# Kernel optimization log

Measured on AMD Instinct MI355X. Metric: run time of the kernel, lower is better.

The kernel has to match this reference:

```python
import jax, jax.numpy as jnp
import numpy as np

N = 100000
NFEAT = 512
NHID = 256
NCLASS = 40
E = 1600000
K = 10          # nlayers propagation hops
ALPHA = 0.1


def setup_inputs() -> dict:
    key = jax.random.key(0)
    ks = jax.random.split(key, 8)
    x = jax.random.normal(ks[0], (N, NFEAT), dtype=jnp.float32)
    edge_src = jax.random.randint(ks[1], (E,), 0, N, dtype=jnp.int32)
    edge_dst = jax.random.randint(ks[2], (E,), 0, N, dtype=jnp.int32)
    # roughly row-stochastic-scale edge values (avg degree ~16)
    edge_val = jax.random.uniform(ks[3], (E,), dtype=jnp.float32) * (1.0 / 16.0)
    stdv1 = 1.0 / np.sqrt(NFEAT)
    W1 = jax.random.uniform(ks[4], (NFEAT, NHID), minval=-stdv1, maxval=stdv1, dtype=jnp.float32)
    b1 = jax.random.uniform(ks[5], (NHID,), minval=-stdv1, maxval=stdv1, dtype=jnp.float32)
    stdv2 = 1.0 / np.sqrt(NHID)
    W2 = jax.random.uniform(ks[6], (NHID, NCLASS), minval=-stdv2, maxval=stdv2, dtype=jnp.float32)
    b2 = jax.random.uniform(ks[7], (NCLASS,), minval=-stdv2, maxval=stdv2, dtype=jnp.float32)
    return {"x": x, "edge_src": edge_src, "edge_dst": edge_dst, "edge_val": edge_val,
            "W1": W1, "b1": b1, "W2": W2, "b2": b2}


def _spmm(edge_src, edge_dst, edge_val, z):
    # sparse adj @ z via gather + segment-sum scatter: out[dst] += val * z[src]
    msgs = edge_val[:, None] * z[edge_src]          # [E, C]
    return jax.ops.segment_sum(msgs, edge_dst, num_segments=N)


def reference(x, edge_src, edge_dst, edge_val, W1, b1, W2, b2):
    # MLP transform (dropout is identity in eval mode)
    h = jax.nn.relu(x @ W1 + b1)                    # [N, NHID]
    h = h @ W2 + b2                                 # [N, NCLASS]
    # APPNP propagation: z <- (1-alpha) * A z + alpha * h
    def step(z, _):
        z = _spmm(edge_src, edge_dst, edge_val, z) * (1.0 - ALPHA) + ALPHA * h
        return z, None
    z, _ = jax.lax.scan(step, h, None, length=K)
    return jax.nn.log_softmax(z, axis=1)
```

## Files before the change

### kernel.cpp

```cpp
#include <hip/hip_runtime.h>
#include <hip/hip_bf16.h>
#include <math.h>

#define NN     100000
#define NFEATD 512
#define NHIDD  256
#define NCLS   40
#define NE     1600000
#define KHOP   10

typedef __attribute__((ext_vector_type(8))) short short8;
typedef __attribute__((ext_vector_type(4))) float floatx4;

static __device__ __forceinline__ float bf2f(unsigned int u) {
  unsigned int x = u << 16;
  float f;
  __builtin_memcpy(&f, &x, 4);
  return f;
}
static __device__ __forceinline__ unsigned short f2bf(float f) {
  unsigned int x;
  __builtin_memcpy(&x, &x, 0);
  __builtin_memcpy(&x, &f, 4);
  x = (x + 0x7fffu + ((x >> 16) & 1u)) >> 16;
  return (unsigned short)x;
}

__global__ __launch_bounds__(256) void wt_kernel(const float* __restrict__ W1,
                                                 unsigned short* __restrict__ Wt) {
  int i = blockIdx.x * 256 + threadIdx.x;
  int k = i >> 8;
  int n = i & 255;
  Wt[n * 512 + k] = f2bf(W1[i]);
}

__global__ __launch_bounds__(256) void gemm1_mfma_kernel(
    const float* __restrict__ x, const unsigned short* __restrict__ Wt,
    const float* __restrict__ b1, unsigned short* __restrict__ h1) {
  __shared__ unsigned short As[128 * 40];
  __shared__ unsigned short Bs[128 * 40];
  const int tid = threadIdx.x;
  const int lane = tid & 63;
  const int wave = tid >> 6;
  const int wr = wave >> 1, wc = wave & 1;
  const int m = lane & 15, quad = lane >> 4;
  const int c0 = blockIdx.x * 128;
  const int r0 = blockIdx.y * 128;

  const int arow = tid >> 3;
  const int akq = tid & 7;
  const int brow = tid >> 2;
  const int bkq = tid & 3;

  floatx4 acc[4][4];
#pragma unroll
  for (int i = 0; i < 4; ++i)
#pragma unroll
    for (int j = 0; j < 4; ++j) acc[i][j] = (floatx4){0.f, 0.f, 0.f, 0.f};

  float4 aR[4];
  uint4 bR[2];
#pragma unroll
  for (int rep = 0; rep < 4; ++rep) {
    int grow = r0 + arow + rep * 32;
    aR[rep] = make_float4(0.f, 0.f, 0.f, 0.f);
    if (grow < NN) aR[rep] = *(const float4*)(x + grow * NFEATD + akq * 4);
  }
#pragma unroll
  for (int rep = 0; rep < 2; ++rep)
    bR[rep] = *(const uint4*)(Wt + (c0 + brow + rep * 64) * NFEATD + bkq * 8);

  for (int kt = 0; kt < NFEATD; kt += 32) {
#pragma unroll
    for (int rep = 0; rep < 4; ++rep) {
      ushort4 o;
      o.x = f2bf(aR[rep].x);
      o.y = f2bf(aR[rep].y);
      o.z = f2bf(aR[rep].z);
      o.w = f2bf(aR[rep].w);
      *(ushort4*)&As[(arow + rep * 32) * 40 + akq * 4] = o;
    }
#pragma unroll
    for (int rep = 0; rep < 2; ++rep)
      *(uint4*)&Bs[(brow + rep * 64) * 40 + bkq * 8] = bR[rep];
    __syncthreads();

    int ktn = kt + 32;
    if (ktn < NFEATD) {
#pragma unroll
      for (int rep = 0; rep < 4; ++rep) {
        int grow = r0 + arow + rep * 32;
        float4 v = make_float4(0.f, 0.f, 0.f, 0.f);
        if (grow < NN) v = *(const float4*)(x + grow * NFEATD + ktn + akq * 4);
        aR[rep] = v;
      }
#pragma unroll
      for (int rep = 0; rep < 2; ++rep)
        bR[rep] = *(const uint4*)(Wt + (c0 + brow + rep * 64) * NFEATD + ktn + bkq * 8);
    }

    short8 af[4], bfr[4];
#pragma unroll
    for (int i = 0; i < 4; ++i)
      af[i] = *(const short8*)&As[(wr * 64 + i * 16 + m) * 40 + quad * 8];
#pragma unroll
    for (int j = 0; j < 4; ++j)
      bfr[j] = *(const short8*)&Bs[(wc * 64 + j * 16 + m) * 40 + quad * 8];
#pragma unroll
    for (int i = 0; i < 4; ++i)
#pragma unroll
      for (int j = 0; j < 4; ++j)
        acc[i][j] = __builtin_amdgcn_mfma_f32_16x16x32_bf16(af[i], bfr[j], acc[i][j], 0, 0, 0);
    __syncthreads();
  }

  float bias[4];
#pragma unroll
  for (int j = 0; j < 4; ++j) bias[j] = b1[c0 + wc * 64 + j * 16 + m];
#pragma unroll
  for (int i = 0; i < 4; ++i) {
#pragma unroll
    for (int r = 0; r < 4; ++r) {
      int row = r0 + wr * 64 + i * 16 + quad * 4 + r;
      if (row < NN) {
#pragma unroll
        for (int j = 0; j < 4; ++j) {
          float v = acc[i][j][r] + bias[j];
          h1[row * NHIDD + c0 + wc * 64 + j * 16 + m] = f2bf(fmaxf(v, 0.f));
        }
      }
    }
  }
}

__global__ __launch_bounds__(256) void gemm2_kernel(
    const unsigned short* __restrict__ h1, const float* __restrict__ W2,
    const float* __restrict__ b2, float* __restrict__ h) {
  __shared__ float w2s[NHIDD * NCLS];
  __shared__ float b2s[NCLS];
  __shared__ unsigned short h1s[64 * 264];
  const int tid = threadIdx.x;
  const int r0 = blockIdx.x * 64;
  for (int i = tid; i < NHIDD * NCLS; i += 256) w2s[i] = W2[i];
  if (tid < NCLS) b2s[tid] = b2[tid];
#pragma unroll
  for (int q = 0; q < 8; ++q) {
    int l = tid + q * 256;
    int lr = l >> 5;
    int lc = (l & 31) << 3;
    int row = r0 + lr;
    uint4 v = make_uint4(0, 0, 0, 0);
    if (row < NN) v = *(const uint4*)(h1 + row * NHIDD + lc);
    *(uint4*)&h1s[lr * 264 + lc] = v;
  }
  __syncthreads();
  const int lr = tid >> 2;
  const int cq = (tid & 3) * 10;
  float acc[10];
#pragma unroll
  for (int j = 0; j < 10; ++j) acc[j] = 0.f;
#pragma unroll 4
  for (int k = 0; k < NHIDD; k += 2) {
    unsigned int hp = *(const unsigned int*)&h1s[lr * 264 + k];
    float a0 = bf2f(hp & 0xffffu);
    float a1 = bf2f(hp >> 16);
    const float* w0 = &w2s[k * NCLS + cq];
    const float* w1 = &w2s[(k + 1) * NCLS + cq];
#pragma unroll
    for (int j = 0; j < 10; ++j)
      acc[j] = fmaf(a1, w1[j], fmaf(a0, w0[j], acc[j]));
  }
  int row = r0 + lr;
  if (row < NN) {
#pragma unroll
    for (int j = 0; j < 10; ++j) h[row * NCLS + cq + j] = acc[j] + b2s[cq + j];
  }
}

__global__ __launch_bounds__(256) void zero_kernel(int* __restrict__ p, int n) {
  int i = blockIdx.x * 256 + threadIdx.x;
  if (i < n) p[i] = 0;
}
__global__ __launch_bounds__(256) void count_kernel(const int* __restrict__ edst,
                                                    int* __restrict__ counts) {
  int e = blockIdx.x * 256 + threadIdx.x;
  if (e < NE) atomicAdd(&counts[edst[e]], 1);
}
__global__ __launch_bounds__(256) void scan_blocks_kernel(
    const int* __restrict__ counts, int* __restrict__ row_start,
    int* __restrict__ bsum) {
  __shared__ int s[256];
  int gid = blockIdx.x * 256 + threadIdx.x;
  int v = (gid < NN) ? counts[gid] : 0;
  s[threadIdx.x] = v;
  __syncthreads();
  for (int off = 1; off < 256; off <<= 1) {
    int t = (threadIdx.x >= off) ? s[threadIdx.x - off] : 0;
    __syncthreads();
    s[threadIdx.x] += t;
    __syncthreads();
  }
  if (gid < NN) row_start[gid + 1] = s[threadIdx.x];
  if (threadIdx.x == 255) bsum[blockIdx.x] = s[255];
}
#define NB 391
__global__ __launch_bounds__(512) void scan_sums_kernel(int* __restrict__ bsum) {
  __shared__ int s[512];
  int tid = threadIdx.x;
  int v = (tid < NB) ? bsum[tid] : 0;
  s[tid] = v;
  __syncthreads();
  for (int off = 1; off < 512; off <<= 1) {
    int t = (tid >= off) ? s[tid - off] : 0;
    __syncthreads();
    s[tid] += t;
    __syncthreads();
  }
  if (tid < NB) bsum[tid] = (tid == 0) ? 0 : s[tid - 1];
}
__global__ __launch_bounds__(256) void add_off_kernel(int* __restrict__ row_start,
                                                      const int* __restrict__ bsum) {
  int gid = blockIdx.x * 256 + threadIdx.x;
  if (gid < NN) row_start[gid + 1] += bsum[blockIdx.x];
  if (gid == 0) row_start[0] = 0;
}
__global__ __launch_bounds__(256) void scatter_kernel(
    const int* __restrict__ esrc, const int* __restrict__ edst,
    const float* __restrict__ eval, const int* __restrict__ row_start,
    int* __restrict__ cursor, int2* __restrict__ csr_pair) {
  int e = blockIdx.x * 256 + threadIdx.x;
  if (e < NE) {
    int d = edst[e];
    int p = atomicAdd(&cursor[d], 1);
    int idx = row_start[d] + p;
    csr_pair[idx] = make_int2(esrc[e], __float_as_int(eval[e]));
  }
}

__global__ __launch_bounds__(256) void prop_kernel(
    const int* __restrict__ row_start, const int2* __restrict__ csr_pair,
    const float* __restrict__ z, const float* __restrict__ h,
    float* __restrict__ zo) {
  int t = blockIdx.x * 256 + threadIdx.x;
  if (t >= NN * 10) return;
  unsigned int r = (unsigned int)t / 10u;
  int cg = t - (int)r * 10;
  const float* zc = z + cg * 4;
  int e0 = row_start[r], e1 = row_start[r + 1];
  float4 acc = make_float4(0.f, 0.f, 0.f, 0.f);
  int e = e0;
  for (; e + 4 <= e1; e += 4) {
    int2 p0 = csr_pair[e + 0];
    int2 p1 = csr_pair[e + 1];
    int2 p2 = csr_pair[e + 2];
    int2 p3 = csr_pair[e + 3];
    const float4 z0 = *(const float4*)(zc + p0.x * 40);
    const float4 z1 = *(const float4*)(zc + p1.x * 40);
    const float4 z2 = *(const float4*)(zc + p2.x * 40);
    const float4 z3 = *(const float4*)(zc + p3.x * 40);
    float v0 = __int_as_float(p0.y), v1 = __int_as_float(p1.y);
    float v2 = __int_as_float(p2.y), v3 = __int_as_float(p3.y);
    acc.x = fmaf(v0, z0.x, acc.x);
    acc.y = fmaf(v0, z0.y, acc.y);
    acc.z = fmaf(v0, z0.z, acc.z);
    acc.w = fmaf(v0, z0.w, acc.w);
    acc.x = fmaf(v1, z1.x, acc.x);
    acc.y = fmaf(v1, z1.y, acc.y);
    acc.z = fmaf(v1, z1.z, acc.z);
    acc.w = fmaf(v1, z1.w, acc.w);
    acc.x = fmaf(v2, z2.x, acc.x);
    acc.y = fmaf(v2, z2.y, acc.y);
    acc.z = fmaf(v2, z2.z, acc.z);
    acc.w = fmaf(v2, z2.w, acc.w);
    acc.x = fmaf(v3, z3.x, acc.x);
    acc.y = fmaf(v3, z3.y, acc.y);
    acc.z = fmaf(v3, z3.z, acc.z);
    acc.w = fmaf(v3, z3.w, acc.w);
  }
  for (; e < e1; ++e) {
    int2 p = csr_pair[e];
    float v = __int_as_float(p.y);
    const float4 zv = *(const float4*)(zc + p.x * 40);
    acc.x = fmaf(v, zv.x, acc.x);
    acc.y = fmaf(v, zv.y, acc.y);
    acc.z = fmaf(v, zv.z, acc.z);
    acc.w = fmaf(v, zv.w, acc.w);
  }
  const float4 hv = *(const float4*)(h + r * NCLS + cg * 4);
  float4 o;
  o.x = 0.9f * acc.x + 0.1f * hv.x;
  o.y = 0.9f * acc.y + 0.1f * hv.y;
  o.z = 0.9f * acc.z + 0.1f * hv.z;
  o.w = 0.9f * acc.w + 0.1f * hv.w;
  *(float4*)(zo + r * NCLS + cg * 4) = o;
}

__global__ __launch_bounds__(256) void lsm_kernel(float* __restrict__ zio) {
  int r = blockIdx.x * 256 + threadIdx.x;
  if (r >= NN) return;
  float v[NCLS];
#pragma unroll
  for (int q = 0; q < 10; ++q) {
    float4 t = *(const float4*)(zio + r * NCLS + q * 4);
    v[q * 4 + 0] = t.x;
    v[q * 4 + 1] = t.y;
    v[q * 4 + 2] = t.z;
    v[q * 4 + 3] = t.w;
  }
  float m = v[0];
#pragma unroll
  for (int i = 1; i < NCLS; ++i) m = fmaxf(m, v[i]);
  float ssum = 0.f;
#pragma unroll
  for (int i = 0; i < NCLS; ++i) ssum += expf(v[i] - m);
  float lse = m + logf(ssum);
#pragma unroll
  for (int q = 0; q < 10; ++q) {
    float4 t;
    t.x = v[q * 4 + 0] - lse;
    t.y = v[q * 4 + 1] - lse;
    t.z = v[q * 4 + 2] - lse;
    t.w = v[q * 4 + 3] - lse;
    *(float4*)(zio + r * NCLS + q * 4) = t;
  }
}

extern "C" void kernel_launch(void* const* d_in, const int* in_sizes, int n_in,
                              void* d_out, int out_size, void* d_ws, size_t ws_size,
                              hipStream_t stream) {
  const float* x = (const float*)d_in[0];
  const int* esrc = (const int*)d_in[1];
  const int* edst = (const int*)d_in[2];
  const float* eval = (const float*)d_in[3];
  const float* W1 = (const float*)d_in[4];
  const float* b1 = (const float*)d_in[5];
  const float* W2 = (const float*)d_in[6];
  const float* b2 = (const float*)d_in[7];
  float* out = (float*)d_out;
  char* ws = (char*)d_ws;

  float* h = (float*)(ws + 0);
  float* zA = (float*)(ws + 16000000);
  unsigned short* Wt = (unsigned short*)(ws + 16000000);
  unsigned short* h1 = (unsigned short*)(ws + 32000000);
  int* counts = (int*)(ws + 83200000);
  int* cursor = (int*)(ws + 83600000);
  int* row_start = (int*)(ws + 84000000);
  int* bsum = (int*)(ws + 84400640);
  int2* csr_pair = (int2*)(ws + 84402688);

  zero_kernel<<<(2 * NN + 255) / 256, 256, 0, stream>>>(counts, 2 * NN);

  wt_kernel<<<(NFEATD * NHIDD) / 256, 256, 0, stream>>>(W1, Wt);
  gemm1_mfma_kernel<<<dim3(2, (NN + 127) / 128), 256, 0, stream>>>(x, Wt, b1, h1);
  gemm2_kernel<<<(NN + 63) / 64, 256, 0, stream>>>(h1, W2, b2, h);

  count_kernel<<<(NE + 255) / 256, 256, 0, stream>>>(edst, counts);
  scan_blocks_kernel<<<NB, 256, 0, stream>>>(counts, row_start, bsum);
  scan_sums_kernel<<<1, 512, 0, stream>>>(bsum);
  add_off_kernel<<<NB, 256, 0, stream>>>(row_start, bsum);
  scatter_kernel<<<(NE + 255) / 256, 256, 0, stream>>>(esrc, edst, eval, row_start,
                                                       cursor, csr_pair);

  const float* zin = h;
  float* zout = zA;
  for (int i = 0; i < KHOP; ++i) {
    prop_kernel<<<(NN * 10 + 255) / 256, 256, 0, stream>>>(row_start, csr_pair,
                                                           zin, h, zout);
    if (i == 0) {
      zin = zA;
      zout = out;
    } else {
      float* t = (float*)zin;
      zin = zout;
      zout = t;
    }
  }

  lsm_kernel<<<(NN + 255) / 256, 256, 0, stream>>>(out);
}
```

Baseline: 1.158 ms.

## Store propagation features in bf16 and degree-sort rows for load balance

The propagation state z and the MLP output h are now stored as bf16 instead of fp32, which halves the bytes gathered per edge in each of the ten SpMM hops. Each thread now handles 8 classes with 16-byte loads, and the edge loop is unrolled by 8. Rows are bucketed by in-degree through a histogram and permutation, and the CSR is built in that sorted order, so neighbouring threads get similar edge counts and wave divergence drops. The cost is a few extra preprocessing kernels, plus bf16 rounding error that builds up across the hops.

```diff
diff --git a/kernel.cpp b/kernel.cpp
--- a/kernel.cpp
+++ b/kernel.cpp
@@ -20,10 +20,21 @@
 }
 static __device__ __forceinline__ unsigned short f2bf(float f) {
   unsigned int x;
-  __builtin_memcpy(&x, &x, 0);
   __builtin_memcpy(&x, &f, 4);
   x = (x + 0x7fffu + ((x >> 16) & 1u)) >> 16;
   return (unsigned short)x;
+}
+static __device__ __forceinline__ void bf8_to_f(const uint4 u, float* f) {
+  unsigned int a0 = u.x, a1 = u.y, a2 = u.z, a3 = u.w;
+  unsigned int t;
+  t = a0 << 16;          __builtin_memcpy(&f[0], &t, 4);
+  t = a0 & 0xffff0000u;  __builtin_memcpy(&f[1], &t, 4);
+  t = a1 << 16;          __builtin_memcpy(&f[2], &t, 4);
+  t = a1 & 0xffff0000u;  __builtin_memcpy(&f[3], &t, 4);
+  t = a2 << 16;          __builtin_memcpy(&f[4], &t, 4);
+  t = a2 & 0xffff0000u;  __builtin_memcpy(&f[5], &t, 4);
+  t = a3 << 16;          __builtin_memcpy(&f[6], &t, 4);
+  t = a3 & 0xffff0000u;  __builtin_memcpy(&f[7], &t, 4);
 }
 
 __global__ __launch_bounds__(256) void wt_kernel(const float* __restrict__ W1,
@@ -135,7 +146,7 @@
 
 __global__ __launch_bounds__(256) void gemm2_kernel(
     const unsigned short* __restrict__ h1, const float* __restrict__ W2,
-    const float* __restrict__ b2, float* __restrict__ h) {
+    const float* __restrict__ b2, unsigned short* __restrict__ hb) {
   __shared__ float w2s[NHIDD * NCLS];
   __shared__ float b2s[NCLS];
   __shared__ unsigned short h1s[64 * 264];
@@ -173,7 +184,11 @@
   int row = r0 + lr;
   if (row < NN) {
 #pragma unroll
-    for (int j = 0; j < 10; ++j) h[row * NCLS + cq + j] = acc[j] + b2s[cq + j];
+    for (int jj = 0; jj < 5; ++jj) {
+      unsigned int u = (unsigned int)f2bf(acc[2 * jj] + b2s[cq + 2 * jj]) |
+                       ((unsigned int)f2bf(acc[2 * jj + 1] + b2s[cq + 2 * jj + 1]) << 16);
+      *(unsigned int*)&hb[row * NCLS + cq + 2 * jj] = u;
+    }
   }
 }
 
@@ -186,12 +201,49 @@
   int e = blockIdx.x * 256 + threadIdx.x;
   if (e < NE) atomicAdd(&counts[edst[e]], 1);
 }
+__global__ __launch_bounds__(256) void hist_kernel(const int* __restrict__ counts,
+                                                   int* __restrict__ binoff) {
+  int r = blockIdx.x * 256 + threadIdx.x;
+  if (r < NN) {
+    int d = counts[r];
+    if (d > 63) d = 63;
+    atomicAdd(&binoff[d], 1);
+  }
+}
+__global__ __launch_bounds__(64) void binscan_kernel(int* __restrict__ binoff) {
+  __shared__ int s[64];
+  int t = threadIdx.x;
+  s[t] = binoff[t];
+  __syncthreads();
+  if (t == 0) {
+    int run = 0;
+    for (int i = 0; i < 64; ++i) {
+      int c = s[i];
+      s[i] = run;
+      run += c;
+    }
+  }
+  __syncthreads();
+  binoff[t] = s[t];
+}
+__global__ __launch_bounds__(256) void scatter_rows_kernel(
+    const int* __restrict__ counts, int* __restrict__ binoff,
+    int* __restrict__ perm, int* __restrict__ spos) {
+  int r = blockIdx.x * 256 + threadIdx.x;
+  if (r < NN) {
+    int d = counts[r];
+    if (d > 63) d = 63;
+    int pos = atomicAdd(&binoff[d], 1);
+    perm[pos] = r;
+    spos[r] = pos;
+  }
+}
 __global__ __launch_bounds__(256) void scan_blocks_kernel(
-    const int* __restrict__ counts, int* __restrict__ row_start,
-    int* __restrict__ bsum) {
+    const int* __restrict__ counts, const int* __restrict__ perm,
+    int* __restrict__ srs, int* __restrict__ bsum) {
   __shared__ int s[256];
   int gid = blockIdx.x * 256 + threadIdx.x;
-  int v = (gid < NN) ? counts[gid] : 0;
+  int v = (gid < NN) ? counts[perm[gid]] : 0;
   s[threadIdx.x] = v;
   __syncthreads();
   for (int off = 1; off < 256; off <<= 1) {
@@ -200,7 +252,7 @@
     s[threadIdx.x] += t;
     __syncthreads();
   }
-  if (gid < NN) row_start[gid + 1] = s[threadIdx.x];
+  if (gid < NN) srs[gid + 1] = s[threadIdx.x];
   if (threadIdx.x == 255) bsum[blockIdx.x] = s[255];
 }
 #define NB 391
@@ -218,94 +270,94 @@
   }
   if (tid < NB) bsum[tid] = (tid == 0) ? 0 : s[tid - 1];
 }
-__global__ __launch_bounds__(256) void add_off_kernel(int* __restrict__ row_start,
+__global__ __launch_bounds__(256) void add_off_kernel(int* __restrict__ srs,
                                                       const int* __restrict__ bsum) {
   int gid = blockIdx.x * 256 + threadIdx.x;
-  if (gid < NN) row_start[gid + 1] += bsum[blockIdx.x];
-  if (gid == 0) row_start[0] = 0;
+  if (gid < NN) srs[gid + 1] += bsum[blockIdx.x];
+  if (gid == 0) srs[0] = 0;
 }
 __global__ __launch_bounds__(256) void scatter_kernel(
     const int* __restrict__ esrc, const int* __restrict__ edst,
-    const float* __restrict__ eval, const int* __restrict__ row_start,
-    int* __restrict__ cursor, int2* __restrict__ csr_pair) {
+    const float* __restrict__ eval, const int* __restrict__ srs,
+    const int* __restrict__ spos, int* __restrict__ cursor,
+    int2* __restrict__ csr_pair) {
   int e = blockIdx.x * 256 + threadIdx.x;
   if (e < NE) {
-    int d = edst[e];
-    int p = atomicAdd(&cursor[d], 1);
-    int idx = row_start[d] + p;
+    int p = spos[edst[e]];
+    int idx = srs[p] + atomicAdd(&cursor[p], 1);
     csr_pair[idx] = make_int2(esrc[e], __float_as_int(eval[e]));
   }
 }
 
 __global__ __launch_bounds__(256) void prop_kernel(
-    const int* __restrict__ row_start, const int2* __restrict__ csr_pair,
-    const float* __restrict__ z, const float* __restrict__ h,
-    float* __restrict__ zo) {
+    const int* __restrict__ srs, const int* __restrict__ perm,
+    const int2* __restrict__ csr_pair, const unsigned short* __restrict__ zi,
+    const unsigned short* __restrict__ hb, unsigned short* __restrict__ zo) {
   int t = blockIdx.x * 256 + threadIdx.x;
-  if (t >= NN * 10) return;
-  unsigned int r = (unsigned int)t / 10u;
-  int cg = t - (int)r * 10;
-  const float* zc = z + cg * 4;
-  int e0 = row_start[r], e1 = row_start[r + 1];
-  float4 acc = make_float4(0.f, 0.f, 0.f, 0.f);
+  if (t >= NN * 5) return;
+  unsigned int p = (unsigned int)t / 5u;
+  int cg8 = (t - (int)p * 5) * 8;
+  int e0 = srs[p], e1 = srs[p + 1];
+  int r = perm[p];
+  float acc[8];
+#pragma unroll
+  for (int j = 0; j < 8; ++j) acc[j] = 0.f;
+
   int e = e0;
-  for (; e + 4 <= e1; e += 4) {
-    int2 p0 = csr_pair[e + 0];
-    int2 p1 = csr_pair[e + 1];
-    int2 p2 = csr_pair[e + 2];
-    int2 p3 = csr_pair[e + 3];
-    const float4 z0 = *(const float4*)(zc + p0.x * 40);
-    const float4 z1 = *(const float4*)(zc + p1.x * 40);
-    const float4 z2 = *(const float4*)(zc + p2.x * 40);
-    const float4 z3 = *(const float4*)(zc + p3.x * 40);
-    float v0 = __int_as_float(p0.y), v1 = __int_as_float(p1.y);
-    float v2 = __int_as_float(p2.y), v3 = __int_as_float(p3.y);
-    acc.x = fmaf(v0, z0.x, acc.x);
-    acc.y = fmaf(v0, z0.y, acc.y);
-    acc.z = fmaf(v0, z0.z, acc.z);
-    acc.w = fmaf(v0, z0.w, acc.w);
-    acc.x = fmaf(v1, z1.x, acc.x);
-    acc.y = fmaf(v1, z1.y, acc.y);
-    acc.z = fmaf(v1, z1.z, acc.z);
-    acc.w = fmaf(v1, z1.w, acc.w);
-    acc.x = fmaf(v2, z2.x, acc.x);
-    acc.y = fmaf(v2, z2.y, acc.y);
-    acc.z = fmaf(v2, z2.z, acc.z);
-    acc.w = fmaf(v2, z2.w, acc.w);
-    acc.x = fmaf(v3, z3.x, acc.x);
-    acc.y = fmaf(v3, z3.y, acc.y);
-    acc.z = fmaf(v3, z3.z, acc.z);
-    acc.w = fmaf(v3, z3.w, acc.w);
+  for (; e + 8 <= e1; e += 8) {
+    int2 pr[8];
+#pragma unroll
+    for (int q = 0; q < 8; ++q) pr[q] = csr_pair[e + q];
+    uint4 g[8];
+#pragma unroll
+    for (int q = 0; q < 8; ++q)
+      g[q] = *(const uint4*)(zi + pr[q].x * NCLS + cg8);
+#pragma unroll
+    for (int q = 0; q < 8; ++q) {
+      float zf[8];
+      bf8_to_f(g[q], zf);
+      float v = __int_as_float(pr[q].y);
+#pragma unroll
+      for (int j = 0; j < 8; ++j) acc[j] = fmaf(v, zf[j], acc[j]);
+    }
   }
   for (; e < e1; ++e) {
-    int2 p = csr_pair[e];
-    float v = __int_as_float(p.y);
-    const float4 zv = *(const float4*)(zc + p.x * 40);
-    acc.x = fmaf(v, zv.x, acc.x);
-    acc.y = fmaf(v, zv.y, acc.y);
-    acc.z = fmaf(v, zv.z, acc.z);
-    acc.w = fmaf(v, zv.w, acc.w);
-  }
-  const float4 hv = *(const float4*)(h + r * NCLS + cg * 4);
-  float4 o;
-  o.x = 0.9f * acc.x + 0.1f * hv.x;
-  o.y = 0.9f * acc.y + 0.1f * hv.y;
-  o.z = 0.9f * acc.z + 0.1f * hv.z;
-  o.w = 0.9f * acc.w + 0.1f * hv.w;
-  *(float4*)(zo + r * NCLS + cg * 4) = o;
-}
-
-__global__ __launch_bounds__(256) void lsm_kernel(float* __restrict__ zio) {
+    int2 pr = csr_pair[e];
+    uint4 g = *(const uint4*)(zi + pr.x * NCLS + cg8);
+    float zf[8];
+    bf8_to_f(g, zf);
+    float v = __int_as_float(pr.y);
+#pragma unroll
+    for (int j = 0; j < 8; ++j) acc[j] = fmaf(v, zf[j], acc[j]);
+  }
+
+  uint4 hu = *(const uint4*)(hb + r * NCLS + cg8);
+  float hf[8];
+  bf8_to_f(hu, hf);
+  uint4 o;
+  unsigned int w[4];
+#pragma unroll
+  for (int i = 0; i < 4; ++i) {
+    unsigned int lo = f2bf(0.9f * acc[2 * i] + 0.1f * hf[2 * i]);
+    unsigned int hi = f2bf(0.9f * acc[2 * i + 1] + 0.1f * hf[2 * i + 1]);
+    w[i] = lo | (hi << 16);
+  }
+  o.x = w[0];
+  o.y = w[1];
+  o.z = w[2];
+  o.w = w[3];
+  *(uint4*)(zo + r * NCLS + cg8) = o;
+}
+
+__global__ __launch_bounds__(256) void lsm_kernel(const unsigned short* __restrict__ zf,
+                                                  float* __restrict__ out) {
   int r = blockIdx.x * 256 + threadIdx.x;
   if (r >= NN) return;
   float v[NCLS];
 #pragma unroll
-  for (int q = 0; q < 10; ++q) {
-    float4 t = *(const float4*)(zio + r * NCLS + q * 4);
-    v[q * 4 + 0] = t.x;
-    v[q * 4 + 1] = t.y;
-    v[q * 4 + 2] = t.z;
-    v[q * 4 + 3] = t.w;
+  for (int q = 0; q < 5; ++q) {
+    uint4 u = *(const uint4*)(zf + r * NCLS + q * 8);
+    bf8_to_f(u, v + q * 8);
   }
   float m = v[0];
 #pragma unroll
@@ -316,12 +368,12 @@
   float lse = m + logf(ssum);
 #pragma unroll
   for (int q = 0; q < 10; ++q) {
-    float4 t;
-    t.x = v[q * 4 + 0] - lse;
-    t.y = v[q * 4 + 1] - lse;
-    t.z = v[q * 4 + 2] - lse;
-    t.w = v[q * 4 + 3] - lse;
-    *(float4*)(zio + r * NCLS + q * 4) = t;
+    float4 o;
+    o.x = v[q * 4 + 0] - lse;
+    o.y = v[q * 4 + 1] - lse;
+    o.z = v[q * 4 + 2] - lse;
+    o.w = v[q * 4 + 3] - lse;
+    *(float4*)(out + r * NCLS + q * 4) = o;
   }
 }
 
@@ -339,43 +391,51 @@
   float* out = (float*)d_out;
   char* ws = (char*)d_ws;
 
-  float* h = (float*)(ws + 0);
-  float* zA = (float*)(ws + 16000000);
-  unsigned short* Wt = (unsigned short*)(ws + 16000000);
-  unsigned short* h1 = (unsigned short*)(ws + 32000000);
-  int* counts = (int*)(ws + 83200000);
-  int* cursor = (int*)(ws + 83600000);
-  int* row_start = (int*)(ws + 84000000);
-  int* bsum = (int*)(ws + 84400640);
-  int2* csr_pair = (int2*)(ws + 84402688);
+  unsigned short* hb = (unsigned short*)(ws + 0);
+  unsigned short* zB0 = (unsigned short*)(ws + 8000000);
+  unsigned short* zB1 = (unsigned short*)(ws + 16000000);
+  unsigned short* Wt = (unsigned short*)(ws + 24000000);
+  unsigned short* h1 = (unsigned short*)(ws + 24400000);
+  int* counts = (int*)(ws + 75600000);
+  int* cursor = (int*)(ws + 76000000);
+  int* srs = (int*)(ws + 76400000);
+  int* bsum = (int*)(ws + 76800064);
+  int* binoff = (int*)(ws + 76802112);
+  int* perm = (int*)(ws + 76802624);
+  int* spos = (int*)(ws + 77202624);
+  int2* csr_pair = (int2*)(ws + 77602624);
 
   zero_kernel<<<(2 * NN + 255) / 256, 256, 0, stream>>>(counts, 2 * NN);
+  zero_kernel<<<1, 256, 0, stream>>>(binoff, 64);
 
   wt_kernel<<<(NFEATD * NHIDD) / 256, 256, 0, stream>>>(W1, Wt);
   gemm1_mfma_kernel<<<dim3(2, (NN + 127) / 128), 256, 0, stream>>>(x, Wt, b1, h1);
-  gemm2_kernel<<<(NN + 63) / 64, 256, 0, stream>>>(h1, W2, b2, h);
+  gemm2_kernel<<<(NN + 63) / 64, 256, 0, stream>>>(h1, W2, b2, hb);
 
   count_kernel<<<(NE + 255) / 256, 256, 0, stream>>>(edst, counts);
-  scan_blocks_kernel<<<NB, 256, 0, stream>>>(counts, row_start, bsum);
+  hist_kernel<<<(NN + 255) / 256, 256, 0, stream>>>(counts, binoff);
+  binscan_kernel<<<1, 64, 0, stream>>>(binoff);
+  scatter_rows_kernel<<<(NN + 255) / 256, 256, 0, stream>>>(counts, binoff, perm, spos);
+  scan_blocks_kernel<<<NB, 256, 0, stream>>>(counts, perm, srs, bsum);
   scan_sums_kernel<<<1, 512, 0, stream>>>(bsum);
-  add_off_kernel<<<NB, 256, 0, stream>>>(row_start, bsum);
-  scatter_kernel<<<(NE + 255) / 256, 256, 0, stream>>>(esrc, edst, eval, row_start,
+  add_off_kernel<<<NB, 256, 0, stream>>>(srs, bsum);
+  scatter_kernel<<<(NE + 255) / 256, 256, 0, stream>>>(esrc, edst, eval, srs, spos,
                                                        cursor, csr_pair);
 
-  const float* zin = h;
-  float* zout = zA;
+  const unsigned short* zin = hb;
+  unsigned short* zout = zB0;
   for (int i = 0; i < KHOP; ++i) {
-    prop_kernel<<<(NN * 10 + 255) / 256, 256, 0, stream>>>(row_start, csr_pair,
-                                                           zin, h, zout);
+    prop_kernel<<<(NN * 5 + 255) / 256, 256, 0, stream>>>(srs, perm, csr_pair,
+                                                          zin, hb, zout);
     if (i == 0) {
-      zin = zA;
-      zout = out;
+      zin = zB0;
+      zout = zB1;
     } else {
-      float* t = (float*)zin;
+      unsigned short* t = (unsigned short*)zin;
       zin = zout;
       zout = t;
     }
   }
 
-  lsm_kernel<<<(NN + 255) / 256, 256, 0, stream>>>(out);
-}
+  lsm_kernel<<<(NN + 255) / 256, 256, 0, stream>>>(zB1, out);
+}
```

Result: slower. 1.450 ms (+25.2%).
